# Performance work log

Hardware: AMD Instinct MI355X
Metric: run time of the kernel (lower is better)

Reference implementation:

```python
import jax, jax.numpy as jnp
import numpy as np

B, N, F_IN, F_OUT = 8, 2048, 128, 64
ALPHA = 0.2  # LeakyReLU negative slope
NEG_BIG = -9e15


def setup_inputs() -> dict:
    key = jax.random.key(0)
    k1, k2, k3, k4 = jax.random.split(key, 4)
    x = jax.random.normal(k1, (B, N, F_IN), dtype=jnp.float32)
    adj = jax.random.randint(k2, (B, N, N), 0, 2, dtype=jnp.int32)
    # xavier-uniform-ish init scale for faithfulness (gain=1.414)
    w_lim = 1.414 * np.sqrt(6.0 / (F_IN + F_OUT))
    a_lim = 1.414 * np.sqrt(6.0 / (2 * F_OUT + 1))
    weight = jax.random.uniform(k3, (F_IN, F_OUT), minval=-w_lim, maxval=w_lim, dtype=jnp.float32)
    weight2 = jax.random.uniform(k4, (2 * F_OUT, 1), minval=-a_lim, maxval=a_lim, dtype=jnp.float32)
    return {"x": x, "adj": adj, "weight": weight, "weight2": weight2}


def reference(x, adj, weight, weight2):
    # Linear projection: [B, N, F_out]
    wh = jnp.einsum("bnf,fo->bno", x, weight)
    # Additive GAT decomposition of concat-score:
    # e_ij = leakyrelu(a1 . Wh_i + a2 . Wh_j)  == original concat @ weight2
    a1 = weight2[:F_OUT, 0]   # [F_out]
    a2 = weight2[F_OUT:, 0]   # [F_out]
    s1 = wh @ a1              # [B, N]
    s2 = wh @ a2              # [B, N]
    e = s1[:, :, None] + s2[:, None, :]          # [B, N, N]
    e = jnp.where(e > 0, e, ALPHA * e)            # LeakyReLU
    e = jnp.where(adj > 0, e, NEG_BIG)            # mask non-edges
    attention = jax.nn.softmax(e, axis=2)         # [B, N, N]
    # dropout is identity in eval mode (training=False)
    out = jnp.einsum("bij,bjo->bio", attention, wh)  # [B, N, F_out]
    return jax.nn.elu(out)
```

## Files before the change

### kernel.cpp

```cpp
#include <hip/hip_runtime.h>
#include <cstdint>
#include <cstddef>

#define B_    8
#define N_    2048
#define FIN   128
#define FOUT  64
#define ALPHA 0.2f
#define NEG_BIG -9.0e15f

typedef __attribute__((ext_vector_type(8))) _Float16 half8;
typedef __attribute__((ext_vector_type(4))) float float4v;

__global__ __launch_bounds__(256, 4) void k1_wh(
    const float* __restrict__ x, const float* __restrict__ W,
    const float* __restrict__ w2, _Float16* __restrict__ whT,
    float* __restrict__ s1, float* __restrict__ s2)
{
    int t = threadIdx.x, lane = t & 63, w = t >> 6;
    float a1 = w2[lane], a2 = w2[FOUT + lane];
    int rowBase = blockIdx.x * 32 + w * 8;
    for (int rr = 0; rr < 8; ++rr) {
        int row = __builtin_amdgcn_readfirstlane(rowBase + rr);
        const float* xr = x + (size_t)row * FIN;
        float acc = 0.f;
        #pragma unroll
        for (int k = 0; k < FIN; ++k)
            acc = fmaf(xr[k], W[k * FOUT + lane], acc);
        int b = row >> 11, j = row & (N_ - 1);
        whT[((size_t)b * FOUT + lane) * N_ + j] = (_Float16)acc;
        float p1 = acc * a1, p2 = acc * a2;
        #pragma unroll
        for (int m = 32; m >= 1; m >>= 1) {
            p1 += __shfl_xor(p1, m);
            p2 += __shfl_xor(p2, m);
        }
        if (lane == 0) { s1[row] = p1; s2[row] = p2; }
    }
}

__global__ __launch_bounds__(256, 4) void k2_attn(
    const int* __restrict__ adj, const _Float16* __restrict__ whT,
    const float* __restrict__ s1, const float* __restrict__ s2,
    float* __restrict__ out)
{
    __shared__ __attribute__((aligned(16))) _Float16 pT[2][16][520];
    __shared__ float lL[16];
    __shared__ float smaxL[4];

    int t = threadIdx.x, lane = t & 63, w = t >> 6;
    int b = blockIdx.x >> 7;
    int i0 = (blockIdx.x & 127) << 4;

    const float4* s2v = (const float4*)(s2 + (size_t)b * N_);
    float4 ua = s2v[t], ub = s2v[t + 256];
    float vm = fmaxf(fmaxf(fmaxf(ua.x, ua.y), fmaxf(ua.z, ua.w)),
                     fmaxf(fmaxf(ub.x, ub.y), fmaxf(ub.z, ub.w)));
    #pragma unroll
    for (int m = 32; m >= 1; m >>= 1) vm = fmaxf(vm, __shfl_xor(vm, m));
    if (lane == 0) smaxL[w] = vm;
    __syncthreads();
    float s2max = fmaxf(fmaxf(smaxL[0], smaxL[1]), fmaxf(smaxL[2], smaxL[3]));

    int l15 = lane & 15, quad = lane >> 4;
    int f0 = w * 16;

    float s1r[4], negmh[4], lacc[4];
    #pragma unroll
    for (int rr = 0; rr < 4; ++rr) {
        float sv = s1[(size_t)b * N_ + i0 + w * 4 + rr];
        float mh = sv + s2max;
        mh = fmaxf(mh, ALPHA * mh);
        s1r[rr] = sv;
        negmh[rr] = -mh;
        lacc[rr] = 0.f;
    }

    const int*      adjB = adj + ((size_t)b * N_ + i0 + w * 4) * N_ + lane * 8;
    const float*    s2B  = s2 + (size_t)b * N_ + lane * 8;
    const _Float16* wB   = whT + ((size_t)b * FOUT + f0 + l15) * N_ + quad * 8;

    float4v acc = {0, 0, 0, 0};

    auto p_phase = [&](int c, int buf) {
        int jc = c * 512;
        const float* s2c = s2B + jc;
        float4 sa = *(const float4*)s2c;
        float4 sb = *(const float4*)(s2c + 4);
        float ss[8] = {sa.x, sa.y, sa.z, sa.w, sb.x, sb.y, sb.z, sb.w};
        #pragma unroll
        for (int rr = 0; rr < 4; ++rr) {
            const int* ap = adjB + (size_t)rr * N_ + jc;
            int4 aj0 = *(const int4*)ap;
            int4 aj1 = *(const int4*)(ap + 4);
            int aa[8] = {aj0.x, aj0.y, aj0.z, aj0.w, aj1.x, aj1.y, aj1.z, aj1.w};
            half8 pf;
            float ls = 0.f;
            #pragma unroll
            for (int e = 0; e < 8; ++e) {
                float v = s1r[rr] + ss[e];
                v = fmaxf(v, ALPHA * v);
                v = (aa[e] > 0) ? v : NEG_BIG;
                float tt = fmaxf(v + negmh[rr], -76.f);
                float p = __expf(tt);
                ls += p;
                pf[e] = (_Float16)p;
            }
            lacc[rr] += ls;
            *(half8*)&pT[buf][w * 4 + rr][lane * 8] = pf;
        }
    };

    p_phase(0, 0);
    __syncthreads();

    #pragma unroll
    for (int c = 0; c < 4; ++c) {
        if (c < 3) {
            p_phase(c + 1, (c + 1) & 1);
        } else {
            #pragma unroll
            for (int rr = 0; rr < 4; ++rr) {
                float v = lacc[rr];
                #pragma unroll
                for (int m = 32; m >= 1; m >>= 1) v += __shfl_xor(v, m);
                if (lane == 0) lL[w * 4 + rr] = v;
            }
        }
        const _Float16* wp = wB + c * 512;
        #pragma unroll
        for (int kk = 0; kk < 16; ++kk) {
            half8 af = *(const half8*)&pT[c & 1][l15][kk * 32 + quad * 8];
            half8 bf = *(const half8*)(wp + kk * 32);
            acc = __builtin_amdgcn_mfma_f32_16x16x32_f16(af, bf, acc, 0, 0, 0);
        }
        __syncthreads();
    }

    #pragma unroll
    for (int reg = 0; reg < 4; ++reg) {
        int row = quad * 4 + reg;
        float val = acc[reg] / lL[row];
        val = (val > 0.f) ? val : (__expf(val) - 1.f);
        out[((size_t)b * N_ + i0 + row) * FOUT + f0 + l15] = val;
    }
}

extern "C" void kernel_launch(void* const* d_in, const int* in_sizes, int n_in,
                              void* d_out, int out_size, void* d_ws, size_t ws_size,
                              hipStream_t stream) {
    const float* x   = (const float*)d_in[0];
    const int*   adj = (const int*)d_in[1];
    const float* W   = (const float*)d_in[2];
    const float* w2  = (const float*)d_in[3];
    float* out = (float*)d_out;

    _Float16* whT = (_Float16*)d_ws;
    float* s1 = (float*)((char*)d_ws + (size_t)B_ * FOUT * N_ * 2);
    float* s2 = s1 + (size_t)B_ * N_;

    k1_wh<<<(B_ * N_) / 32, 256, 0, stream>>>(x, W, w2, whT, s1, s2);
    k2_attn<<<(B_ * N_) / 16, 256, 0, stream>>>(adj, whT, s1, s2, out);
}
```

Before: 265.8 us.

## Single-buffer P tile, prefetch whT fragments early, and interleave batches across blocks

Replaces the double-buffered P tile in shared memory with a single buffer and restructures the chunk loop. For each chunk, the first half of the whT B-fragments and all adj loads are issued before the exp/softmax work, and the second half is loaded after the barrier, so global latency is hidden by register prefetch instead of LDS double-buffering. Block-to-batch mapping is changed so consecutive blocks take different batches, and launch bounds drop to 3 waves per SIMD to allow more registers. The trade-off is an extra barrier per chunk and lower occupancy in exchange for more in-flight loads.

```diff
diff --git a/kernel.cpp b/kernel.cpp
--- a/kernel.cpp
+++ b/kernel.cpp
@@ -39,18 +39,18 @@
     }
 }
 
-__global__ __launch_bounds__(256, 4) void k2_attn(
+__global__ __launch_bounds__(256, 3) void k2_attn(
     const int* __restrict__ adj, const _Float16* __restrict__ whT,
     const float* __restrict__ s1, const float* __restrict__ s2,
     float* __restrict__ out)
 {
-    __shared__ __attribute__((aligned(16))) _Float16 pT[2][16][520];
+    __shared__ __attribute__((aligned(16))) _Float16 pT[16][520];
     __shared__ float lL[16];
     __shared__ float smaxL[4];
 
     int t = threadIdx.x, lane = t & 63, w = t >> 6;
-    int b = blockIdx.x >> 7;
-    int i0 = (blockIdx.x & 127) << 4;
+    int b = blockIdx.x & 7;
+    int i0 = (blockIdx.x >> 3) << 4;
 
     const float4* s2v = (const float4*)(s2 + (size_t)b * N_);
     float4 ua = s2v[t], ub = s2v[t + 256];
@@ -82,18 +82,32 @@
 
     float4v acc = {0, 0, 0, 0};
 
-    auto p_phase = [&](int c, int buf) {
-        int jc = c * 512;
+    #pragma unroll
+    for (int c = 0; c < 4; ++c) {
+        const int jc = c * 512;
+        const _Float16* wp = wB + jc;
+
+        half8 bfr0[8];
+        #pragma unroll
+        for (int kk = 0; kk < 8; ++kk)
+            bfr0[kk] = *(const half8*)(wp + kk * 32);
+
+        int4 aj[4][2];
+        #pragma unroll
+        for (int rr = 0; rr < 4; ++rr) {
+            const int* ap = adjB + (size_t)rr * N_ + jc;
+            aj[rr][0] = *(const int4*)ap;
+            aj[rr][1] = *(const int4*)(ap + 4);
+        }
         const float* s2c = s2B + jc;
         float4 sa = *(const float4*)s2c;
         float4 sb = *(const float4*)(s2c + 4);
         float ss[8] = {sa.x, sa.y, sa.z, sa.w, sb.x, sb.y, sb.z, sb.w};
+
         #pragma unroll
         for (int rr = 0; rr < 4; ++rr) {
-            const int* ap = adjB + (size_t)rr * N_ + jc;
-            int4 aj0 = *(const int4*)ap;
-            int4 aj1 = *(const int4*)(ap + 4);
-            int aa[8] = {aj0.x, aj0.y, aj0.z, aj0.w, aj1.x, aj1.y, aj1.z, aj1.w};
+            int aa[8] = {aj[rr][0].x, aj[rr][0].y, aj[rr][0].z, aj[rr][0].w,
+                         aj[rr][1].x, aj[rr][1].y, aj[rr][1].z, aj[rr][1].w};
             half8 pf;
             float ls = 0.f;
             #pragma unroll
@@ -107,18 +121,10 @@
                 pf[e] = (_Float16)p;
             }
             lacc[rr] += ls;
-            *(half8*)&pT[buf][w * 4 + rr][lane * 8] = pf;
+            *(half8*)&pT[w * 4 + rr][lane * 8] = pf;
         }
-    };
 
-    p_phase(0, 0);
-    __syncthreads();
-
-    #pragma unroll
-    for (int c = 0; c < 4; ++c) {
-        if (c < 3) {
-            p_phase(c + 1, (c + 1) & 1);
-        } else {
+        if (c == 3) {
             #pragma unroll
             for (int rr = 0; rr < 4; ++rr) {
                 float v = lacc[rr];
@@ -127,12 +133,22 @@
                 if (lane == 0) lL[w * 4 + rr] = v;
             }
         }
-        const _Float16* wp = wB + c * 512;
+        __syncthreads();
+
+        half8 bfr1[8];
         #pragma unroll
-        for (int kk = 0; kk < 16; ++kk) {
-            half8 af = *(const half8*)&pT[c & 1][l15][kk * 32 + quad * 8];
-            half8 bf = *(const half8*)(wp + kk * 32);
-            acc = __builtin_amdgcn_mfma_f32_16x16x32_f16(af, bf, acc, 0, 0, 0);
+        for (int kk = 0; kk < 8; ++kk)
+            bfr1[kk] = *(const half8*)(wp + (kk + 8) * 32);
+
+        #pragma unroll
+        for (int kk = 0; kk < 8; ++kk) {
+            half8 af = *(const half8*)&pT[l15][kk * 32 + quad * 8];
+            acc = __builtin_amdgcn_mfma_f32_16x16x32_f16(af, bfr0[kk], acc, 0, 0, 0);
+        }
+        #pragma unroll
+        for (int kk = 0; kk < 8; ++kk) {
+            half8 af = *(const half8*)&pT[l15][(kk + 8) * 32 + quad * 8];
+            acc = __builtin_amdgcn_mfma_f32_16x16x32_f16(af, bfr1[kk], acc, 0, 0, 0);
         }
         __syncthreads();
     }
```

New measurement: 283.9 us. 6.8% more time.
